# Performance work log

Hardware: AMD Instinct MI355X
Metric: run time of the kernel (lower is better)

## Reference

```python
import jax, jax.numpy as jnp
import numpy as np

B, N, DIM = 8, 1024, 768
HEADS, DHEAD = 12, 64
INNER = HEADS * DHEAD  # 768
ALPHA = 0.25
SCALE = DHEAD ** -0.5
EPS = 1e-5


def setup_inputs() -> dict:
    key = jax.random.key(0)
    ks = jax.random.split(key, 7)
    x = jax.random.normal(ks[0], (B, N, DIM), dtype=jnp.float32)
    h = jax.random.normal(ks[1], (B, HEADS, N, N), dtype=jnp.float32)
    gamma = jnp.ones((DIM,), dtype=jnp.float32)
    beta = jnp.zeros((DIM,), dtype=jnp.float32)
    w_qkv = jax.random.normal(ks[2], (DIM, 3 * INNER), dtype=jnp.float32) * (DIM ** -0.5)
    w_out = jax.random.normal(ks[3], (INNER, DIM), dtype=jnp.float32) * (INNER ** -0.5)
    b_out = jnp.zeros((DIM,), dtype=jnp.float32)
    return {"x": x, "h": h, "gamma": gamma, "beta": beta,
            "w_qkv": w_qkv, "w_out": w_out, "b_out": b_out}


def reference(x, h, gamma, beta, w_qkv, w_out, b_out):
    # LayerNorm over last dim
    mu = jnp.mean(x, axis=-1, keepdims=True)
    var = jnp.mean(jnp.square(x - mu), axis=-1, keepdims=True)
    xn = (x - mu) * jax.lax.rsqrt(var + EPS) * gamma + beta
    # fused QKV projection (no bias)
    qkv = xn @ w_qkv                                     # (b, n, 3*inner)
    q, k, v = jnp.split(qkv, 3, axis=-1)
    split_heads = lambda t: t.reshape(B, N, HEADS, DHEAD).transpose(0, 2, 1, 3)  # b h n d
    q, k, v = split_heads(q), split_heads(k), split_heads(v)
    raw = jnp.einsum('bhid,bhjd->bhij', q, k) * SCALE    # (b, h, n, n)
    blended = ALPHA * raw + (1.0 - ALPHA) * h
    attn = jax.nn.softmax(blended, axis=-1)              # dropout p=0 -> identity
    out = jnp.einsum('bhij,bhjd->bhid', attn, v)         # (b, h, n, d)
    out = out.transpose(0, 2, 1, 3).reshape(B, N, INNER)
    out = out @ w_out + b_out
    return (out, blended)
```

## Files before the change

kernel.cpp:

```cpp
#include <hip/hip_runtime.h>
#include <hip/hip_bf16.h>
#include <stdint.h>

#define NB 8
#define NSEQ 1024
#define DIMM 768
#define NHEADS 12
#define DH 64
#define NQKV 2304
#define ALPHA_ 0.25f
#define SCALE_ 0.125f
#define EPS_ 1e-5f

typedef __bf16 bf16;
typedef bf16 bf16x8 __attribute__((ext_vector_type(8)));
typedef bf16 bf16x4 __attribute__((ext_vector_type(4)));
typedef float f32x4 __attribute__((ext_vector_type(4)));

#define MFMA16(a, b, c) __builtin_amdgcn_mfma_f32_16x16x32_bf16((a), (b), (c), 0, 0, 0)

static __device__ __forceinline__ void load_lds16(const void* gsrc, void* ldst) {
  __builtin_amdgcn_global_load_lds(
      (__attribute__((address_space(1))) void*)gsrc,
      (__attribute__((address_space(3))) void*)ldst, 16, 0, 0);
}

__global__ __launch_bounds__(256) void ln_kernel(
    const float* __restrict__ x, const float* __restrict__ gamma,
    const float* __restrict__ beta, bf16* __restrict__ xn) {
  const int row = blockIdx.x * 4 + (threadIdx.x >> 6);
  const int lane = threadIdx.x & 63;
  const float* xr = x + (size_t)row * DIMM;
  float4 v[3];
  float s = 0.f, s2 = 0.f;
#pragma unroll
  for (int c = 0; c < 3; ++c) {
    v[c] = *reinterpret_cast<const float4*>(xr + c * 256 + lane * 4);
    s += v[c].x + v[c].y + v[c].z + v[c].w;
    s2 += v[c].x * v[c].x + v[c].y * v[c].y + v[c].z * v[c].z + v[c].w * v[c].w;
  }
#pragma unroll
  for (int m = 1; m < 64; m <<= 1) {
    s += __shfl_xor(s, m);
    s2 += __shfl_xor(s2, m);
  }
  const float mu = s * (1.f / DIMM);
  const float rstd = rsqrtf(s2 * (1.f / DIMM) - mu * mu + EPS_);
#pragma unroll
  for (int c = 0; c < 3; ++c) {
    const float4 g4 = *reinterpret_cast<const float4*>(gamma + c * 256 + lane * 4);
    const float4 b4 = *reinterpret_cast<const float4*>(beta + c * 256 + lane * 4);
    bf16x4 o;
    o[0] = (bf16)((v[c].x - mu) * rstd * g4.x + b4.x);
    o[1] = (bf16)((v[c].y - mu) * rstd * g4.y + b4.y);
    o[2] = (bf16)((v[c].z - mu) * rstd * g4.z + b4.z);
    o[3] = (bf16)((v[c].w - mu) * rstd * g4.w + b4.w);
    *reinterpret_cast<bf16x4*>(xn + (size_t)row * DIMM + c * 256 + lane * 4) = o;
  }
}

__global__ __launch_bounds__(256) void tcast_kernel(
    const float* __restrict__ in, bf16* __restrict__ out, int R, int C) {
  __shared__ float tile[32][33];
  const int tx = threadIdx.x & 31, ty = threadIdx.x >> 5;
  const int c0 = blockIdx.x * 32, r0 = blockIdx.y * 32;
#pragma unroll
  for (int i = ty; i < 32; i += 8)
    tile[i][tx] = in[(size_t)(r0 + i) * C + c0 + tx];
  __syncthreads();
#pragma unroll
  for (int i = ty; i < 32; i += 8)
    out[(size_t)(c0 + i) * R + r0 + tx] = (bf16)tile[tx][i];
}

__global__ __launch_bounds__(256) void qkv_gemm(
    const bf16* __restrict__ xn, const bf16* __restrict__ wT,
    bf16* __restrict__ qb, bf16* __restrict__ kb, bf16* __restrict__ vt) {
  __shared__ __align__(16) bf16 As[128 * 32];
  __shared__ __align__(16) bf16 Bs[64 * 32];
  const int tid = threadIdx.x;
  const int wv = tid >> 6, l = tid & 63;
  const int l16 = l & 15, q4 = l >> 4;
  const int c0 = blockIdx.x * 64, row0 = blockIdx.y * 128;
  const int sr = tid >> 2, skk = (tid & 3) * 8;
  f32x4 acc0[4], acc1[4];
#pragma unroll
  for (int c = 0; c < 4; ++c) {
    acc0[c] = f32x4{0.f, 0.f, 0.f, 0.f};
    acc1[c] = f32x4{0.f, 0.f, 0.f, 0.f};
  }
  for (int k0 = 0; k0 < DIMM; k0 += 32) {
    __syncthreads();
    load_lds16(xn + (size_t)(row0 + sr) * DIMM + k0 + skk, As + tid * 8);
    load_lds16(xn + (size_t)(row0 + 64 + sr) * DIMM + k0 + skk, As + 2048 + tid * 8);
    load_lds16(wT + (size_t)(c0 + sr) * DIMM + k0 + skk, Bs + tid * 8);
    __syncthreads();
    const bf16x8 a0 = *reinterpret_cast<const bf16x8*>(&As[(wv * 32 + l16) * 32 + q4 * 8]);
    const bf16x8 a1 = *reinterpret_cast<const bf16x8*>(&As[(wv * 32 + 16 + l16) * 32 + q4 * 8]);
#pragma unroll
    for (int c = 0; c < 4; ++c) {
      const bf16x8 bb = *reinterpret_cast<const bf16x8*>(&Bs[(c * 16 + l16) * 32 + q4 * 8]);
      acc0[c] = MFMA16(a0, bb, acc0[c]);
      acc1[c] = MFMA16(a1, bb, acc1[c]);
    }
  }
  const int sect = c0 / DIMM;
  const int head = (c0 % DIMM) >> 6;
#pragma unroll
  for (int c = 0; c < 4; ++c) {
    const int dd = c * 16 + l16;
#pragma unroll
    for (int r = 0; r < 4; ++r) {
#pragma unroll
      for (int rsub = 0; rsub < 2; ++rsub) {
        const int gm = row0 + wv * 32 + rsub * 16 + q4 * 4 + r;
        const int b = gm >> 10, n = gm & 1023;
        const size_t bhh = (size_t)b * NHEADS + head;
        const float av = rsub ? acc1[c][r] : acc0[c][r];
        const bf16 val = (bf16)av;
        if (sect == 0)      qb[(bhh * NSEQ + n) * DH + dd] = val;
        else if (sect == 1) kb[(bhh * NSEQ + n) * DH + dd] = val;
        else                vt[(bhh * DH + dd) * NSEQ + n] = val;
      }
    }
  }
}

__global__ __launch_bounds__(256) void attn_kernel(
    const bf16* __restrict__ qb, const bf16* __restrict__ kb,
    const bf16* __restrict__ vt, const float* __restrict__ h,
    float* __restrict__ blended, bf16* __restrict__ attn_out) {
  __shared__ __align__(16) bf16 plds[4][16 * 64];
  const int tid = threadIdx.x;
  const int wv = tid >> 6, l = tid & 63;
  const int l16 = l & 15, q4 = l >> 4;
  const int i0 = blockIdx.x * 64 + wv * 16;
  const int bh = blockIdx.y;
  const float* hrow = h + ((size_t)bh << 20);
  float* brow = blended + ((size_t)bh << 20);
  const bf16* kbase = kb + (size_t)bh * NSEQ * DH;
  const bf16* vbase = vt + (size_t)bh * DH * NSEQ;

  bf16x8 aq[2];
#pragma unroll
  for (int w2 = 0; w2 < 2; ++w2)
    aq[w2] = *reinterpret_cast<const bf16x8*>(
        qb + ((size_t)bh * NSEQ + i0 + l16) * DH + w2 * 32 + q4 * 8);

  f32x4 acc[4];
  float m_run[4], l_run[4];
#pragma unroll
  for (int r = 0; r < 4; ++r) { m_run[r] = -1e30f; l_run[r] = 0.f; }
#pragma unroll
  for (int f = 0; f < 4; ++f) acc[f] = f32x4{0.f, 0.f, 0.f, 0.f};

  bf16* pw = plds[wv];

  for (int jt = 0; jt < 16; ++jt) {
    const int j0 = jt * 64;
    f32x4 s[4];
#pragma unroll
    for (int js = 0; js < 4; ++js) s[js] = f32x4{0.f, 0.f, 0.f, 0.f};
#pragma unroll
    for (int js = 0; js < 4; ++js) {
#pragma unroll
      for (int w2 = 0; w2 < 2; ++w2) {
        const bf16x8 kf = *reinterpret_cast<const bf16x8*>(
            kbase + (size_t)(j0 + js * 16 + l16) * DH + w2 * 32 + q4 * 8);
        s[js] = MFMA16(aq[w2], kf, s[js]);
      }
    }
    float bl[4][4];
    float tmax[4] = {-1e30f, -1e30f, -1e30f, -1e30f};
#pragma unroll
    for (int js = 0; js < 4; ++js) {
#pragma unroll
      for (int r = 0; r < 4; ++r) {
        const int gi = i0 + q4 * 4 + r;
        const size_t off = (size_t)gi * NSEQ + j0 + js * 16 + l16;
        const float hv = hrow[off];
        const float val = s[js][r] * (ALPHA_ * SCALE_) + 0.75f * hv;
        brow[off] = val;
        bl[js][r] = val;
        tmax[r] = fmaxf(tmax[r], val);
      }
    }
#pragma unroll
    for (int r = 0; r < 4; ++r) {
#pragma unroll
      for (int mm = 1; mm < 16; mm <<= 1)
        tmax[r] = fmaxf(tmax[r], __shfl_xor(tmax[r], mm));
    }
    float rsum[4] = {0.f, 0.f, 0.f, 0.f};
#pragma unroll
    for (int r = 0; r < 4; ++r) {
      const float mnew = fmaxf(m_run[r], tmax[r]);
      const float sc = __expf(m_run[r] - mnew);
      m_run[r] = mnew;
      l_run[r] *= sc;
#pragma unroll
      for (int f = 0; f < 4; ++f) acc[f][r] *= sc;
      const int prow = q4 * 4 + r;
#pragma unroll
      for (int js = 0; js < 4; ++js) {
        const float p = __expf(bl[js][r] - mnew);
        rsum[r] += p;
        const int blk = (js * 2 + (l16 >> 3)) ^ (prow & 7);
        pw[prow * 64 + blk * 8 + (l16 & 7)] = (bf16)p;
      }
    }
#pragma unroll
    for (int r = 0; r < 4; ++r) {
      float rs = rsum[r];
#pragma unroll
      for (int mm = 1; mm < 16; mm <<= 1) rs += __shfl_xor(rs, mm);
      l_run[r] += rs;
    }
    __syncthreads();
    bf16x8 pa[2];
#pragma unroll
    for (int w2 = 0; w2 < 2; ++w2) {
      const int blk = (w2 * 4 + q4) ^ (l16 & 7);
      pa[w2] = *reinterpret_cast<const bf16x8*>(&pw[l16 * 64 + blk * 8]);
    }
#pragma unroll
    for (int f = 0; f < 4; ++f) {
#pragma unroll
      for (int w2 = 0; w2 < 2; ++w2) {
        const bf16x8 vf = *reinterpret_cast<const bf16x8*>(
            vbase + (size_t)(f * 16 + l16) * NSEQ + j0 + w2 * 32 + q4 * 8);
        acc[f] = MFMA16(pa[w2], vf, acc[f]);
      }
    }
    __syncthreads();
  }
  const int b = bh / NHEADS, head = bh % NHEADS;
  float inv[4];
#pragma unroll
  for (int r = 0; r < 4; ++r) inv[r] = 1.f / l_run[r];
#pragma unroll
  for (int f = 0; f < 4; ++f) {
#pragma unroll
    for (int r = 0; r < 4; ++r) {
      const int gi = i0 + q4 * 4 + r;
      attn_out[((size_t)b * NSEQ + gi) * DIMM + head * DH + f * 16 + l16] =
          (bf16)(acc[f][r] * inv[r]);
    }
  }
}

__global__ __launch_bounds__(256) void oproj_gemm(
    const bf16* __restrict__ ain, const bf16* __restrict__ wT,
    const float* __restrict__ bias, float* __restrict__ out) {
  __shared__ __align__(16) bf16 As[128 * 32];
  __shared__ __align__(16) bf16 Bs[64 * 32];
  const int tid = threadIdx.x;
  const int wv = tid >> 6, l = tid & 63;
  const int l16 = l & 15, q4 = l >> 4;
  const int c0 = blockIdx.x * 64, row0 = blockIdx.y * 128;
  const int sr = tid >> 2, skk = (tid & 3) * 8;
  f32x4 acc0[4], acc1[4];
#pragma unroll
  for (int c = 0; c < 4; ++c) {
    acc0[c] = f32x4{0.f, 0.f, 0.f, 0.f};
    acc1[c] = f32x4{0.f, 0.f, 0.f, 0.f};
  }
  for (int k0 = 0; k0 < DIMM; k0 += 32) {
    __syncthreads();
    load_lds16(ain + (size_t)(row0 + sr) * DIMM + k0 + skk, As + tid * 8);
    load_lds16(ain + (size_t)(row0 + 64 + sr) * DIMM + k0 + skk, As + 2048 + tid * 8);
    load_lds16(wT + (size_t)(c0 + sr) * DIMM + k0 + skk, Bs + tid * 8);
    __syncthreads();
    const bf16x8 a0 = *reinterpret_cast<const bf16x8*>(&As[(wv * 32 + l16) * 32 + q4 * 8]);
    const bf16x8 a1 = *reinterpret_cast<const bf16x8*>(&As[(wv * 32 + 16 + l16) * 32 + q4 * 8]);
#pragma unroll
    for (int c = 0; c < 4; ++c) {
      const bf16x8 bb = *reinterpret_cast<const bf16x8*>(&Bs[(c * 16 + l16) * 32 + q4 * 8]);
      acc0[c] = MFMA16(a0, bb, acc0[c]);
      acc1[c] = MFMA16(a1, bb, acc1[c]);
    }
  }
#pragma unroll
  for (int c = 0; c < 4; ++c) {
    const int gc = c0 + c * 16 + l16;
    const float bv = bias[gc];
#pragma unroll
    for (int r = 0; r < 4; ++r) {
      out[(size_t)(row0 + wv * 32 + q4 * 4 + r) * DIMM + gc] = acc0[c][r] + bv;
      out[(size_t)(row0 + wv * 32 + 16 + q4 * 4 + r) * DIMM + gc] = acc1[c][r] + bv;
    }
  }
}

extern "C" void kernel_launch(void* const* d_in, const int* in_sizes, int n_in,
                              void* d_out, int out_size, void* d_ws, size_t ws_size,
                              hipStream_t stream) {
  const float* x = (const float*)d_in[0];
  const float* h = (const float*)d_in[1];
  const float* gamma = (const float*)d_in[2];
  const float* beta = (const float*)d_in[3];
  const float* w_qkv = (const float*)d_in[4];
  const float* w_out = (const float*)d_in[5];
  const float* b_out = (const float*)d_in[6];
  float* out = (float*)d_out;
  float* blended = out + (size_t)NB * NSEQ * DIMM;

  char* ws = (char*)d_ws;
  bf16* xn = (bf16*)(ws);
  bf16* qb = (bf16*)(ws + 12582912);
  bf16* kb = (bf16*)(ws + 25165824);
  bf16* vt = (bf16*)(ws + 37748736);
  bf16* wqkvT = (bf16*)(ws + 50331648);
  bf16* woutT = (bf16*)(ws + 53870592);

  hipLaunchKernelGGL(ln_kernel, dim3(2048), dim3(256), 0, stream, x, gamma, beta, xn);
  hipLaunchKernelGGL(tcast_kernel, dim3(72, 24), dim3(256), 0, stream, w_qkv, wqkvT, DIMM, NQKV);
  hipLaunchKernelGGL(tcast_kernel, dim3(24, 24), dim3(256), 0, stream, w_out, woutT, DIMM, DIMM);
  hipLaunchKernelGGL(qkv_gemm, dim3(36, 64), dim3(256), 0, stream, xn, wqkvT, qb, kb, vt);
  hipLaunchKernelGGL(attn_kernel, dim3(16, 96), dim3(256), 0, stream, qb, kb, vt, h, blended, xn);
  hipLaunchKernelGGL(oproj_gemm, dim3(12, 64), dim3(256), 0, stream, xn, woutT, b_out, out);
}
```

Measured before the change: 453.9 us.

## Double-buffer h tile loads in registers and drop block-level barriers

The attention loop is split into a LOADH step and a BODY step and manually unrolled by two. The h tile for the next key block is loaded into a second register buffer while the current block is processed, hiding global-load latency on the large h stream. Both __syncthreads calls are removed, since each wave only touches its own LDS slice and in-order LDS access within a wave is enough. The h and blended pointers are precomputed per lane. The cost is 32 extra VGPRs for the two h buffers, which may lower occupancy.

```diff
diff --git a/kernel.cpp b/kernel.cpp
--- a/kernel.cpp
+++ b/kernel.cpp
@@ -136,8 +136,8 @@
   const int l16 = l & 15, q4 = l >> 4;
   const int i0 = blockIdx.x * 64 + wv * 16;
   const int bh = blockIdx.y;
-  const float* hrow = h + ((size_t)bh << 20);
-  float* brow = blended + ((size_t)bh << 20);
+  const float* hbase = h + ((size_t)bh << 20) + (size_t)(i0 + q4 * 4) * NSEQ + l16;
+  float* bbase = blended + ((size_t)bh << 20) + (size_t)(i0 + q4 * 4) * NSEQ + l16;
   const bf16* kbase = kb + (size_t)bh * NSEQ * DH;
   const bf16* vbase = vt + (size_t)bh * DH * NSEQ;
 
@@ -156,7 +156,15 @@
 
   bf16* pw = plds[wv];
 
-  for (int jt = 0; jt < 16; ++jt) {
+  auto LOADH = [&](int jt, float* dst) {
+#pragma unroll
+    for (int js = 0; js < 4; ++js)
+#pragma unroll
+      for (int r = 0; r < 4; ++r)
+        dst[js * 4 + r] = hbase[(size_t)r * NSEQ + jt * 64 + js * 16];
+  };
+
+  auto BODY = [&](int jt, const float* hc) {
     const int j0 = jt * 64;
     f32x4 s[4];
 #pragma unroll
@@ -176,11 +184,8 @@
     for (int js = 0; js < 4; ++js) {
 #pragma unroll
       for (int r = 0; r < 4; ++r) {
-        const int gi = i0 + q4 * 4 + r;
-        const size_t off = (size_t)gi * NSEQ + j0 + js * 16 + l16;
-        const float hv = hrow[off];
-        const float val = s[js][r] * (ALPHA_ * SCALE_) + 0.75f * hv;
-        brow[off] = val;
+        const float val = s[js][r] * (ALPHA_ * SCALE_) + 0.75f * hc[js * 4 + r];
+        bbase[(size_t)r * NSEQ + j0 + js * 16] = val;
         bl[js][r] = val;
         tmax[r] = fmaxf(tmax[r], val);
       }
@@ -216,7 +221,6 @@
       for (int mm = 1; mm < 16; mm <<= 1) rs += __shfl_xor(rs, mm);
       l_run[r] += rs;
     }
-    __syncthreads();
     bf16x8 pa[2];
 #pragma unroll
     for (int w2 = 0; w2 < 2; ++w2) {
@@ -232,8 +236,17 @@
         acc[f] = MFMA16(pa[w2], vf, acc[f]);
       }
     }
-    __syncthreads();
-  }
+  };
+
+  float hA[16], hB[16];
+  LOADH(0, hA);
+  for (int jt = 0; jt < 16; jt += 2) {
+    LOADH(jt + 1, hB);
+    BODY(jt, hA);
+    if (jt + 2 < 16) LOADH(jt + 2, hA);
+    BODY(jt + 1, hB);
+  }
+
   const int b = bh / NHEADS, head = bh % NHEADS;
   float inv[4];
 #pragma unroll
```

Result: slower. 465.1 us (+2.5%).

## Split attention keys across waves and stage h tiles through LDS asynchronously

Applied to the files above, without the earlier changes.

Each attention block now owns 16 query rows, and its four waves each take a quarter of every 256-key tile. Row max and row sum are combined across waves through shared memory, and the partial outputs are reduced at the end. The h tile is double-buffered into LDS with global_load_lds and updated in place, then written to blended as fully coalesced float4 rows. The aim is to replace scattered 64-byte h reads and blended writes with wide async transfers. In exchange, every block rereads the whole K and V for only 16 rows, and each tile adds extra barriers.

```diff
diff --git a/kernel.cpp b/kernel.cpp
--- a/kernel.cpp
+++ b/kernel.cpp
@@ -24,6 +24,22 @@
       (__attribute__((address_space(1))) void*)gsrc,
       (__attribute__((address_space(3))) void*)ldst, 16, 0, 0);
 }
+
+#define BAR_LGKM()                                             \
+  do {                                                         \
+    __builtin_amdgcn_sched_barrier(0);                         \
+    asm volatile("s_waitcnt lgkmcnt(0)" ::: "memory");         \
+    __builtin_amdgcn_s_barrier();                              \
+    __builtin_amdgcn_sched_barrier(0);                         \
+  } while (0)
+
+#define BAR_FULL()                                                   \
+  do {                                                               \
+    __builtin_amdgcn_sched_barrier(0);                               \
+    asm volatile("s_waitcnt vmcnt(0) lgkmcnt(0)" ::: "memory");      \
+    __builtin_amdgcn_s_barrier();                                    \
+    __builtin_amdgcn_sched_barrier(0);                               \
+  } while (0)
 
 __global__ __launch_bounds__(256) void ln_kernel(
     const float* __restrict__ x, const float* __restrict__ gamma,
@@ -130,16 +146,22 @@
     const bf16* __restrict__ qb, const bf16* __restrict__ kb,
     const bf16* __restrict__ vt, const float* __restrict__ h,
     float* __restrict__ blended, bf16* __restrict__ attn_out) {
-  __shared__ __align__(16) bf16 plds[4][16 * 64];
+  __shared__ __align__(16) float h_lds[2][16][260];
+  __shared__ __align__(16) bf16 pw_all[4][16 * 64];
+  __shared__ float wred_max[4][16];
+  __shared__ float wred_sum[4][16];
+  __shared__ float lfin[16];
+
   const int tid = threadIdx.x;
   const int wv = tid >> 6, l = tid & 63;
   const int l16 = l & 15, q4 = l >> 4;
-  const int i0 = blockIdx.x * 64 + wv * 16;
+  const int i0 = blockIdx.x * 16;
   const int bh = blockIdx.y;
   const float* hrow = h + ((size_t)bh << 20);
   float* brow = blended + ((size_t)bh << 20);
   const bf16* kbase = kb + (size_t)bh * NSEQ * DH;
   const bf16* vbase = vt + (size_t)bh * DH * NSEQ;
+  const int jc0 = wv * 64;
 
   bf16x8 aq[2];
 #pragma unroll
@@ -154,10 +176,23 @@
 #pragma unroll
   for (int f = 0; f < 4; ++f) acc[f] = f32x4{0.f, 0.f, 0.f, 0.f};
 
-  bf16* pw = plds[wv];
-
-  for (int jt = 0; jt < 16; ++jt) {
-    const int j0 = jt * 64;
+  bf16* pw = pw_all[wv];
+
+  auto STAGE = [&](int jtn, int nb) {
+#pragma unroll
+    for (int c = 0; c < 4; ++c) {
+      const int row = wv * 4 + c;
+      load_lds16(hrow + (size_t)(i0 + row) * NSEQ + jtn * 256 + l * 4,
+                 &h_lds[nb][row][0]);
+    }
+  };
+
+  STAGE(0, 0);
+
+  for (int jt = 0; jt < 4; ++jt) {
+    const int cur = jt & 1;
+    const int j0 = jt * 256 + jc0;
+
     f32x4 s[4];
 #pragma unroll
     for (int js = 0; js < 4; ++js) s[js] = f32x4{0.f, 0.f, 0.f, 0.f};
@@ -170,17 +205,20 @@
         s[js] = MFMA16(aq[w2], kf, s[js]);
       }
     }
+
+    BAR_FULL();
+
+    if (jt < 3) STAGE(jt + 1, cur ^ 1);
+
     float bl[4][4];
     float tmax[4] = {-1e30f, -1e30f, -1e30f, -1e30f};
 #pragma unroll
     for (int js = 0; js < 4; ++js) {
 #pragma unroll
       for (int r = 0; r < 4; ++r) {
-        const int gi = i0 + q4 * 4 + r;
-        const size_t off = (size_t)gi * NSEQ + j0 + js * 16 + l16;
-        const float hv = hrow[off];
-        const float val = s[js][r] * (ALPHA_ * SCALE_) + 0.75f * hv;
-        brow[off] = val;
+        float* hp = &h_lds[cur][q4 * 4 + r][jc0 + js * 16 + l16];
+        const float val = s[js][r] * (ALPHA_ * SCALE_) + 0.75f * (*hp);
+        *hp = val;
         bl[js][r] = val;
         tmax[r] = fmaxf(tmax[r], val);
       }
@@ -191,22 +229,31 @@
       for (int mm = 1; mm < 16; mm <<= 1)
         tmax[r] = fmaxf(tmax[r], __shfl_xor(tmax[r], mm));
     }
-    float rsum[4] = {0.f, 0.f, 0.f, 0.f};
-#pragma unroll
-    for (int r = 0; r < 4; ++r) {
-      const float mnew = fmaxf(m_run[r], tmax[r]);
+    if (l16 == 0) {
+#pragma unroll
+      for (int r = 0; r < 4; ++r) wred_max[wv][q4 * 4 + r] = tmax[r];
+    }
+    BAR_LGKM();
+
+    float rsum[4];
+#pragma unroll
+    for (int r = 0; r < 4; ++r) {
+      const int row = q4 * 4 + r;
+      const float mt = fmaxf(fmaxf(wred_max[0][row], wred_max[1][row]),
+                             fmaxf(wred_max[2][row], wred_max[3][row]));
+      const float mnew = fmaxf(m_run[r], mt);
       const float sc = __expf(m_run[r] - mnew);
       m_run[r] = mnew;
       l_run[r] *= sc;
 #pragma unroll
       for (int f = 0; f < 4; ++f) acc[f][r] *= sc;
-      const int prow = q4 * 4 + r;
+      rsum[r] = 0.f;
 #pragma unroll
       for (int js = 0; js < 4; ++js) {
         const float p = __expf(bl[js][r] - mnew);
         rsum[r] += p;
-        const int blk = (js * 2 + (l16 >> 3)) ^ (prow & 7);
-        pw[prow * 64 + blk * 8 + (l16 & 7)] = (bf16)p;
+        const int blk = (js * 2 + (l16 >> 3)) ^ (row & 7);
+        pw[row * 64 + blk * 8 + (l16 & 7)] = (bf16)p;
       }
     }
 #pragma unroll
@@ -214,9 +261,16 @@
       float rs = rsum[r];
 #pragma unroll
       for (int mm = 1; mm < 16; mm <<= 1) rs += __shfl_xor(rs, mm);
-      l_run[r] += rs;
-    }
-    __syncthreads();
+      if (l16 == 0) wred_sum[wv][q4 * 4 + r] = rs;
+    }
+    BAR_LGKM();
+
+#pragma unroll
+    for (int r = 0; r < 4; ++r) {
+      const int row = q4 * 4 + r;
+      l_run[r] += wred_sum[0][row] + wred_sum[1][row] +
+                  wred_sum[2][row] + wred_sum[3][row];
+    }
     bf16x8 pa[2];
 #pragma unroll
     for (int w2 = 0; w2 < 2; ++w2) {
@@ -228,24 +282,39 @@
 #pragma unroll
       for (int w2 = 0; w2 < 2; ++w2) {
         const bf16x8 vf = *reinterpret_cast<const bf16x8*>(
-            vbase + (size_t)(f * 16 + l16) * NSEQ + j0 + w2 * 32 + q4 * 8);
+            vbase + (size_t)(f * 16 + l16) * NSEQ + jt * 256 + jc0 + w2 * 32 + q4 * 8);
         acc[f] = MFMA16(pa[w2], vf, acc[f]);
       }
     }
-    __syncthreads();
-  }
+
+#pragma unroll
+    for (int c = 0; c < 4; ++c) {
+      const int row = wv * 4 + c;
+      const float4 vv = *reinterpret_cast<const float4*>(&h_lds[cur][row][l * 4]);
+      *reinterpret_cast<float4*>(brow + (size_t)(i0 + row) * NSEQ + jt * 256 + l * 4) = vv;
+    }
+  }
+
+  if (wv == 0 && l16 == 0) {
+#pragma unroll
+    for (int r = 0; r < 4; ++r) lfin[q4 * 4 + r] = l_run[r];
+  }
+  float* ored = &h_lds[0][0][0];
+#pragma unroll
+  for (int f = 0; f < 4; ++f) {
+#pragma unroll
+    for (int r = 0; r < 4; ++r)
+      ored[(wv * 16 + q4 * 4 + r) * 64 + f * 16 + l16] = acc[f][r];
+  }
+  BAR_LGKM();
   const int b = bh / NHEADS, head = bh % NHEADS;
-  float inv[4];
-#pragma unroll
-  for (int r = 0; r < 4; ++r) inv[r] = 1.f / l_run[r];
-#pragma unroll
-  for (int f = 0; f < 4; ++f) {
-#pragma unroll
-    for (int r = 0; r < 4; ++r) {
-      const int gi = i0 + q4 * 4 + r;
-      attn_out[((size_t)b * NSEQ + gi) * DIMM + head * DH + f * 16 + l16] =
-          (bf16)(acc[f][r] * inv[r]);
-    }
+#pragma unroll
+  for (int c = 0; c < 4; ++c) {
+    const int row = wv * 4 + c;
+    float o = ored[(0 * 16 + row) * 64 + l] + ored[(1 * 16 + row) * 64 + l] +
+              ored[(2 * 16 + row) * 64 + l] + ored[(3 * 16 + row) * 64 + l];
+    o *= 1.f / lfin[row];
+    attn_out[((size_t)b * NSEQ + i0 + row) * DIMM + head * DH + l] = (bf16)o;
   }
 }
 
@@ -317,6 +386,6 @@
   hipLaunchKernelGGL(tcast_kernel, dim3(72, 24), dim3(256), 0, stream, w_qkv, wqkvT, DIMM, NQKV);
   hipLaunchKernelGGL(tcast_kernel, dim3(24, 24), dim3(256), 0, stream, w_out, woutT, DIMM, DIMM);
   hipLaunchKernelGGL(qkv_gemm, dim3(36, 64), dim3(256), 0, stream, xn, wqkvT, qb, kb, vt);
-  hipLaunchKernelGGL(attn_kernel, dim3(16, 96), dim3(256), 0, stream, qb, kb, vt, h, blended, xn);
+  hipLaunchKernelGGL(attn_kernel, dim3(64, 96), dim3(256), 0, stream, qb, kb, vt, h, blended, xn);
   hipLaunchKernelGGL(oproj_gemm, dim3(12, 64), dim3(256), 0, stream, xn, woutT, b_out, out);
 }
```

After: 397.7 us. 1.14x faster.

## Split attention KV range across waves with transposed MFMA and cross-wave merge

Applied to the files above, without the earlier changes.

Each block now handles 16 query rows, and its four waves each process a quarter of the key range (split-K flash attention). The waves' partial softmax statistics and outputs are merged through LDS at the end. The MFMA operands are swapped so each lane holds contiguous columns, which allows float4 loads of h and float4 stores of blended, with the next tile's h prefetched into registers. The per-tile __syncthreads are removed, and the grid grows from 16x96 to 64x96 blocks. The aim is more memory-level parallelism and wider transactions on the dominant h/blended traffic, at the cost of a cross-wave reduction and reloading K and V in every block.

```diff
diff --git a/kernel.cpp b/kernel.cpp
--- a/kernel.cpp
+++ b/kernel.cpp
@@ -126,38 +126,45 @@
   }
 }
 
-__global__ __launch_bounds__(256) void attn_kernel(
+__global__ __launch_bounds__(256, 4) void attn_kernel(
     const bf16* __restrict__ qb, const bf16* __restrict__ kb,
     const bf16* __restrict__ vt, const float* __restrict__ h,
     float* __restrict__ blended, bf16* __restrict__ attn_out) {
-  __shared__ __align__(16) bf16 plds[4][16 * 64];
+  __shared__ __align__(16) bf16 pw_all[4][16][80];
+  __shared__ __align__(16) float ored[4][16][68];
+  __shared__ float wred_m[4][16];
+  __shared__ float wred_l[4][16];
+
   const int tid = threadIdx.x;
   const int wv = tid >> 6, l = tid & 63;
   const int l16 = l & 15, q4 = l >> 4;
-  const int i0 = blockIdx.x * 64 + wv * 16;
+  const int i0 = blockIdx.x * 16;
   const int bh = blockIdx.y;
-  const float* hrow = h + ((size_t)bh << 20);
-  float* brow = blended + ((size_t)bh << 20);
-  const bf16* kbase = kb + (size_t)bh * NSEQ * DH;
-  const bf16* vbase = vt + (size_t)bh * DH * NSEQ;
-
-  bf16x8 aq[2];
+  const int jb = wv * 256;
+
+  const float* hq = h + ((size_t)bh << 20) + (size_t)(i0 + l16) * NSEQ + jb + q4 * 4;
+  float* bq = blended + ((size_t)bh << 20) + (size_t)(i0 + l16) * NSEQ + jb + q4 * 4;
+  const bf16* kq = kb + ((size_t)bh * NSEQ + jb + l16) * DH + q4 * 8;
+  const bf16* vq = vt + ((size_t)bh * DH + l16) * NSEQ + jb + q4 * 8;
+  bf16(*pw)[80] = pw_all[wv];
+
+  bf16x8 qT[2];
 #pragma unroll
   for (int w2 = 0; w2 < 2; ++w2)
-    aq[w2] = *reinterpret_cast<const bf16x8*>(
+    qT[w2] = *reinterpret_cast<const bf16x8*>(
         qb + ((size_t)bh * NSEQ + i0 + l16) * DH + w2 * 32 + q4 * 8);
 
+  float m_run = -1e30f, l_run = 0.f;
   f32x4 acc[4];
-  float m_run[4], l_run[4];
-#pragma unroll
-  for (int r = 0; r < 4; ++r) { m_run[r] = -1e30f; l_run[r] = 0.f; }
 #pragma unroll
   for (int f = 0; f < 4; ++f) acc[f] = f32x4{0.f, 0.f, 0.f, 0.f};
 
-  bf16* pw = plds[wv];
-
-  for (int jt = 0; jt < 16; ++jt) {
-    const int j0 = jt * 64;
+  float4 hvA[4], hvB[4];
+#pragma unroll
+  for (int js = 0; js < 4; ++js)
+    hvA[js] = *reinterpret_cast<const float4*>(hq + js * 16);
+
+  auto BODY = [&](int st, float4* hcur, float4* hnext, bool pf) {
     f32x4 s[4];
 #pragma unroll
     for (int js = 0; js < 4; ++js) s[js] = f32x4{0.f, 0.f, 0.f, 0.f};
@@ -166,86 +173,101 @@
 #pragma unroll
       for (int w2 = 0; w2 < 2; ++w2) {
         const bf16x8 kf = *reinterpret_cast<const bf16x8*>(
-            kbase + (size_t)(j0 + js * 16 + l16) * DH + w2 * 32 + q4 * 8);
-        s[js] = MFMA16(aq[w2], kf, s[js]);
+            kq + (size_t)(st * 64 + js * 16) * DH + w2 * 32);
+        s[js] = MFMA16(kf, qT[w2], s[js]);
       }
     }
-    float bl[4][4];
-    float tmax[4] = {-1e30f, -1e30f, -1e30f, -1e30f};
+    if (pf) {
+#pragma unroll
+      for (int js = 0; js < 4; ++js)
+        hnext[js] = *reinterpret_cast<const float4*>(hq + (st + 1) * 64 + js * 16);
+    }
+    float tm = -1e30f;
 #pragma unroll
     for (int js = 0; js < 4; ++js) {
+      float4 b;
+      b.x = s[js][0] * (ALPHA_ * SCALE_) + 0.75f * hcur[js].x;
+      b.y = s[js][1] * (ALPHA_ * SCALE_) + 0.75f * hcur[js].y;
+      b.z = s[js][2] * (ALPHA_ * SCALE_) + 0.75f * hcur[js].z;
+      b.w = s[js][3] * (ALPHA_ * SCALE_) + 0.75f * hcur[js].w;
+      *reinterpret_cast<float4*>(bq + st * 64 + js * 16) = b;
+      s[js][0] = b.x; s[js][1] = b.y; s[js][2] = b.z; s[js][3] = b.w;
+      tm = fmaxf(tm, fmaxf(fmaxf(b.x, b.y), fmaxf(b.z, b.w)));
+    }
+    tm = fmaxf(tm, __shfl_xor(tm, 16));
+    tm = fmaxf(tm, __shfl_xor(tm, 32));
+    const float mnew = fmaxf(m_run, tm);
+    const float sc = __expf(m_run - mnew);
+    m_run = mnew;
+    l_run *= sc;
+#pragma unroll
+    for (int f = 0; f < 4; ++f) acc[f] *= sc;
+    float rs = 0.f;
+#pragma unroll
+    for (int js = 0; js < 4; ++js) {
+      bf16x4 pk;
 #pragma unroll
       for (int r = 0; r < 4; ++r) {
-        const int gi = i0 + q4 * 4 + r;
-        const size_t off = (size_t)gi * NSEQ + j0 + js * 16 + l16;
-        const float hv = hrow[off];
-        const float val = s[js][r] * (ALPHA_ * SCALE_) + 0.75f * hv;
-        brow[off] = val;
-        bl[js][r] = val;
-        tmax[r] = fmaxf(tmax[r], val);
+        const float p = __expf(s[js][r] - mnew);
+        rs += p;
+        pk[r] = (bf16)p;
       }
-    }
-#pragma unroll
-    for (int r = 0; r < 4; ++r) {
-#pragma unroll
-      for (int mm = 1; mm < 16; mm <<= 1)
-        tmax[r] = fmaxf(tmax[r], __shfl_xor(tmax[r], mm));
-    }
-    float rsum[4] = {0.f, 0.f, 0.f, 0.f};
-#pragma unroll
-    for (int r = 0; r < 4; ++r) {
-      const float mnew = fmaxf(m_run[r], tmax[r]);
-      const float sc = __expf(m_run[r] - mnew);
-      m_run[r] = mnew;
-      l_run[r] *= sc;
-#pragma unroll
-      for (int f = 0; f < 4; ++f) acc[f][r] *= sc;
-      const int prow = q4 * 4 + r;
-#pragma unroll
-      for (int js = 0; js < 4; ++js) {
-        const float p = __expf(bl[js][r] - mnew);
-        rsum[r] += p;
-        const int blk = (js * 2 + (l16 >> 3)) ^ (prow & 7);
-        pw[prow * 64 + blk * 8 + (l16 & 7)] = (bf16)p;
-      }
-    }
-#pragma unroll
-    for (int r = 0; r < 4; ++r) {
-      float rs = rsum[r];
-#pragma unroll
-      for (int mm = 1; mm < 16; mm <<= 1) rs += __shfl_xor(rs, mm);
-      l_run[r] += rs;
-    }
-    __syncthreads();
+      *reinterpret_cast<bf16x4*>(&pw[l16][js * 16 + q4 * 4]) = pk;
+    }
+    rs += __shfl_xor(rs, 16);
+    rs += __shfl_xor(rs, 32);
+    l_run += rs;
     bf16x8 pa[2];
 #pragma unroll
-    for (int w2 = 0; w2 < 2; ++w2) {
-      const int blk = (w2 * 4 + q4) ^ (l16 & 7);
-      pa[w2] = *reinterpret_cast<const bf16x8*>(&pw[l16 * 64 + blk * 8]);
-    }
+    for (int w2 = 0; w2 < 2; ++w2)
+      pa[w2] = *reinterpret_cast<const bf16x8*>(&pw[l16][w2 * 32 + q4 * 8]);
 #pragma unroll
     for (int f = 0; f < 4; ++f) {
 #pragma unroll
       for (int w2 = 0; w2 < 2; ++w2) {
         const bf16x8 vf = *reinterpret_cast<const bf16x8*>(
-            vbase + (size_t)(f * 16 + l16) * NSEQ + j0 + w2 * 32 + q4 * 8);
-        acc[f] = MFMA16(pa[w2], vf, acc[f]);
+            vq + (size_t)(f * 16) * NSEQ + st * 64 + w2 * 32);
+        acc[f] = MFMA16(vf, pa[w2], acc[f]);
       }
     }
-    __syncthreads();
-  }
+  };
+
+  BODY(0, hvA, hvB, true);
+  BODY(1, hvB, hvA, true);
+  BODY(2, hvA, hvB, true);
+  BODY(3, hvB, hvA, false);
+
+  if (q4 == 0) {
+    wred_m[wv][l16] = m_run;
+    wred_l[wv][l16] = l_run;
+  }
+  __syncthreads();
+  float ms = -1e30f;
+#pragma unroll
+  for (int w = 0; w < 4; ++w) ms = fmaxf(ms, wred_m[w][l16]);
+  float ls = 0.f;
+#pragma unroll
+  for (int w = 0; w < 4; ++w) ls += wred_l[w][l16] * __expf(wred_m[w][l16] - ms);
+  const float osc = __expf(m_run - ms) / ls;
+#pragma unroll
+  for (int f = 0; f < 4; ++f) {
+    f32x4 sv = acc[f] * osc;
+    *reinterpret_cast<f32x4*>(&ored[wv][l16][f * 16 + q4 * 4]) = sv;
+  }
+  __syncthreads();
   const int b = bh / NHEADS, head = bh % NHEADS;
-  float inv[4];
-#pragma unroll
-  for (int r = 0; r < 4; ++r) inv[r] = 1.f / l_run[r];
-#pragma unroll
-  for (int f = 0; f < 4; ++f) {
-#pragma unroll
-    for (int r = 0; r < 4; ++r) {
-      const int gi = i0 + q4 * 4 + r;
-      attn_out[((size_t)b * NSEQ + gi) * DIMM + head * DH + f * 16 + l16] =
-          (bf16)(acc[f][r] * inv[r]);
-    }
+#pragma unroll
+  for (int m = 0; m < 4; ++m) {
+    float4 o = *reinterpret_cast<const float4*>(&ored[0][l16][q4 * 16 + 4 * m]);
+#pragma unroll
+    for (int w = 1; w < 4; ++w) {
+      const float4 t = *reinterpret_cast<const float4*>(&ored[w][l16][q4 * 16 + 4 * m]);
+      o.x += t.x; o.y += t.y; o.z += t.z; o.w += t.w;
+    }
+    bf16x4 ov;
+    ov[0] = (bf16)o.x; ov[1] = (bf16)o.y; ov[2] = (bf16)o.z; ov[3] = (bf16)o.w;
+    *reinterpret_cast<bf16x4*>(
+        attn_out + ((size_t)b * NSEQ + i0 + l16) * DIMM + head * DH + q4 * 16 + 4 * m) = ov;
   }
 }
 
@@ -317,6 +339,6 @@
   hipLaunchKernelGGL(tcast_kernel, dim3(72, 24), dim3(256), 0, stream, w_qkv, wqkvT, DIMM, NQKV);
   hipLaunchKernelGGL(tcast_kernel, dim3(24, 24), dim3(256), 0, stream, w_out, woutT, DIMM, DIMM);
   hipLaunchKernelGGL(qkv_gemm, dim3(36, 64), dim3(256), 0, stream, xn, wqkvT, qb, kb, vt);
-  hipLaunchKernelGGL(attn_kernel, dim3(16, 96), dim3(256), 0, stream, qb, kb, vt, h, blended, xn);
+  hipLaunchKernelGGL(attn_kernel, dim3(64, 96), dim3(256), 0, stream, qb, kb, vt, h, blended, xn);
   hipLaunchKernelGGL(oproj_gemm, dim3(12, 64), dim3(256), 0, stream, xn, woutT, b_out, out);
 }
```

Result: slower. 468.3 us (+3.2%).
